# Kernel tuning notes

Hardware: AMD Instinct MI355X
Metric: run time of the kernel (lower is better)

The kernel has to match this reference:

```python
import jax, jax.numpy as jnp
import numpy as np

M1 = 16
M2 = 16

def _spectral_conv(x, w1c, w2c):
    # x: [B,C,H,W] real; w*c: [C,C,M1,M2] complex
    B, C, H, W = x.shape
    xft = jnp.fft.rfft2(x)                      # [B,C,H,W//2+1]
    top = jnp.einsum('bixy,ioxy->boxy', xft[:, :, :M1, :M2], w1c)
    bot = jnp.einsum('bixy,ioxy->boxy', xft[:, :, -M1:, :M2], w2c)
    out_ft = jnp.zeros((B, w1c.shape[1], H, W // 2 + 1), dtype=xft.dtype)
    out_ft = out_ft.at[:, :, :M1, :M2].set(top)
    out_ft = out_ft.at[:, :, -M1:, :M2].set(bot)
    return jnp.fft.irfft2(out_ft, s=(H, W))

def _fourier_layer(x, w1c, w2c, cw, cb):
    x1 = _spectral_conv(x, w1c, w2c)
    x2 = jnp.einsum('bchw,oc->bohw', x, cw) + cb[None, :, None, None]  # 1x1 conv
    return jax.nn.gelu(x1 + x2, approximate=False)

def setup_inputs() -> dict:
    key = jax.random.key(0)
    ks = jax.random.split(key, 12)
    B, H, W, Tin, C, step = 8, 256, 256, 10, 32, 5
    scale = 1.0 / (C * C)
    return {
        'x': jax.random.normal(ks[0], (B, H, W, Tin), dtype=jnp.float32),
        'fc0_w': jax.random.normal(ks[1], (Tin + 2, C), dtype=jnp.float32) * 0.1,
        'fc0_b': jax.random.normal(ks[2], (C,), dtype=jnp.float32) * 0.1,
        'w1': jax.random.uniform(ks[3], (6, C, C, M1, M2, 2), dtype=jnp.float32) * scale,
        'w2': jax.random.uniform(ks[4], (6, C, C, M1, M2, 2), dtype=jnp.float32) * scale,
        'conv_w': jax.random.normal(ks[5], (6, C, C), dtype=jnp.float32) * 0.1,
        'conv_b': jax.random.normal(ks[6], (6, C), dtype=jnp.float32) * 0.1,
        'fc1_w': jax.random.normal(ks[7], (C, 128), dtype=jnp.float32) * 0.1,
        'fc1_b': jax.random.normal(ks[8], (128,), dtype=jnp.float32) * 0.1,
        'fc2_w': jax.random.normal(ks[9], (128, step), dtype=jnp.float32) * 0.1,
        'fc2_b': jax.random.normal(ks[10], (step,), dtype=jnp.float32) * 0.1,
    }

def reference(x, fc0_w, fc0_b, w1, w2, conv_w, conv_b, fc1_w, fc1_b, fc2_w, fc2_b):
    B, H, W, _ = x.shape
    gridx = jnp.broadcast_to(jnp.linspace(0.0, 1.0, H, dtype=x.dtype)[None, :, None, None], (B, H, W, 1))
    gridy = jnp.broadcast_to(jnp.linspace(0.0, 1.0, W, dtype=x.dtype)[None, None, :, None], (B, H, W, 1))
    h = jnp.concatenate([x, gridx, gridy], axis=-1)          # [B,H,W,T_in+2]
    h = jnp.einsum('bhwc,cd->bhwd', h, fc0_w) + fc0_b        # lift
    h = jnp.transpose(h, (0, 3, 1, 2))                        # [B,C,H,W]
    w1c = jax.lax.complex(w1[..., 0], w1[..., 1])
    w2c = jax.lax.complex(w2[..., 0], w2[..., 1])
    f = lambda z, i: _fourier_layer(z, w1c[i], w2c[i], conv_w[i], conv_b[i])
    h0 = f(h, 0)
    h = f(h, 1)
    h = f(h, 2) + h0
    h1 = f(h, 3)
    h = f(h, 4)
    h = f(h, 5) + h1
    h = jnp.transpose(h, (0, 2, 3, 1))                        # [B,H,W,C]
    h = jax.nn.gelu(jnp.einsum('bhwc,cd->bhwd', h, fc1_w) + fc1_b, approximate=False)
    return jnp.einsum('bhwc,cd->bhwd', h, fc2_w) + fc2_b      # [B,H,W,step]
```

## Files before the change

### kernel.cpp

```cpp
#include <hip/hip_runtime.h>
#include <math.h>

#define C_ 32
#define H_ 256
#define W_ 256
#define HW_ 65536
#define CHW_ 2097152
#define TWO_PI 6.28318530717958647692f

typedef __bf16 bf16x8 __attribute__((ext_vector_type(8)));
typedef float  f32x4  __attribute__((ext_vector_type(4)));

__device__ __forceinline__ bf16x8 as_bf16x8(uint4 u) {
    return __builtin_bit_cast(bf16x8, u);
}
__device__ __forceinline__ unsigned short bfbits(__bf16 h) {
    return __builtin_bit_cast(unsigned short, h);
}
__device__ __forceinline__ bf16x8 mk8(unsigned a, unsigned b, unsigned c, unsigned d) {
    return __builtin_bit_cast(bf16x8, make_uint4(a, b, c, d));
}
__device__ __forceinline__ unsigned rot16(unsigned v) { return (v >> 16) | (v << 16); }
__device__ __forceinline__ uint2 splitpack(float x, float y) {
    __bf16 xh = (__bf16)x, yh = (__bf16)y;
    float xl = x - (float)xh, yl = y - (float)yh;
    unsigned hi = (unsigned)bfbits(xh) | ((unsigned)bfbits(yh) << 16);
    unsigned lo = (unsigned)bfbits((__bf16)xl) | ((unsigned)bfbits((__bf16)yl) << 16);
    return make_uint2(hi, lo);
}

__device__ __forceinline__ float gelu_exact(float x) {
    return 0.5f * x * (1.0f + erff(x * 0.7071067811865475f));
}

__global__ void k_probe(float* __restrict__ out, float ws_kib) {
    if (threadIdx.x == 0 && blockIdx.x == 0) out[0] = ws_kib;
}

__global__ __launch_bounds__(256)
void k_twprep(unsigned short* __restrict__ twfg, uint2* __restrict__ twbfg,
              float2* __restrict__ twg) {
    int f = blockIdx.x * 256 + threadIdx.x;
    {
        int i  = f & 7;
        int c  = (f >> 3) & 15;
        int g  = (f >> 7) & 3;
        int nt = (f >> 9) & 1;
        int kk = f >> 10;
        int k  = kk * 32 + 8 * g + i;
        int a  = (k * c) & 255;
        float ang = (float)a * (TWO_PI / 256.0f);
        float s_, c_; sincosf(ang, &s_, &c_);
        float val = nt ? -s_ : c_;
        __bf16 hi = (__bf16)val;
        __bf16 lo = (__bf16)(val - (float)hi);
        twfg[f]        = bfbits(hi);
        twfg[8192 + f] = bfbits(lo);
    }
    if (f < 256) {
        float a = TWO_PI * (1.0f / 256.0f) * (float)f;
        float s_, c_; sincosf(a, &s_, &c_);
        twbfg[f] = splitpack(c_, s_);
        twg[f]   = make_float2(c_, s_);
    }
}

__global__ __launch_bounds__(256)
void k_lift(const float* __restrict__ xb, const float* __restrict__ fc0_w,
            const float* __restrict__ fc0_b, float* __restrict__ out) {
    __shared__ float wsh[12 * 32];
    __shared__ float bsh[32];
    int tid = threadIdx.x;
    for (int n = tid; n < 384; n += 256) wsh[n] = fc0_w[n];
    if (tid < 32) bsh[tid] = fc0_b[tid];
    __syncthreads();
    int p = blockIdx.x * 256 + tid;
    int w = p & 255;
    int h = (p >> 8) & 255;
    float in[12];
    const float* xp = xb + (size_t)p * 10;
    #pragma unroll
    for (int t = 0; t < 10; ++t) in[t] = xp[t];
    in[10] = (float)h * (1.0f / 255.0f);
    in[11] = (float)w * (1.0f / 255.0f);
    float* op = out + (p & 0xFFFF) + (size_t)(p >> 16) * CHW_;
    #pragma unroll
    for (int c = 0; c < 32; ++c) {
        float acc = bsh[c];
        #pragma unroll
        for (int t = 0; t < 12; ++t) acc += in[t] * wsh[t * 32 + c];
        op[(size_t)c * HW_] = acc;
    }
}

__global__ __launch_bounds__(512)
void k_dftw_dfth(const float* __restrict__ X, float* __restrict__ G,
                 const unsigned short* __restrict__ twfg,
                 const uint2* __restrict__ twbfg) {
    __shared__ __align__(16) unsigned short twf[16384];
    __shared__ uint2 twbf[256];
    __shared__ uint2 slp[256][17];
    int tid = threadIdx.x;
    {
        const uint4* tf4 = (const uint4*)twfg;
        uint4* tw4 = (uint4*)twf;
        #pragma unroll
        for (int f = tid; f < 2048; f += 512) tw4[f] = tf4[f];
        if (tid < 256) twbf[tid] = twbfg[tid];
    }
    __syncthreads();
    int wv = tid >> 6, lane = tid & 63, kg = lane >> 4, cl = lane & 15;
    const uint4* twp = (const uint4*)twf;
    int bo = blockIdx.x;
    const float* xp = X + (size_t)bo * HW_;
    #pragma unroll
    for (int tt = 0; tt < 2; ++tt) {
        int t = wv * 2 + tt;
        const float* xr = xp + (size_t)(t * 16 + cl) * 256 + 8 * kg;
        f32x4 acc0 = {0.f, 0.f, 0.f, 0.f};
        f32x4 acc1 = {0.f, 0.f, 0.f, 0.f};
        #pragma unroll
        for (int kk = 0; kk < 8; ++kk) {
            float4 a0 = *(const float4*)(xr + kk * 32);
            float4 a1 = *(const float4*)(xr + kk * 32 + 4);
            float xv[8] = {a0.x, a0.y, a0.z, a0.w, a1.x, a1.y, a1.z, a1.w};
            bf16x8 Ah, Al;
            #pragma unroll
            for (int i = 0; i < 8; ++i) {
                __bf16 h = (__bf16)xv[i];
                Ah[i] = h;
                Al[i] = (__bf16)(xv[i] - (float)h);
            }
            int base = kk * 128 + kg * 16 + cl;
            bf16x8 Bh0 = as_bf16x8(twp[base]);
            bf16x8 Bh1 = as_bf16x8(twp[base + 64]);
            bf16x8 Bl0 = as_bf16x8(twp[base + 1024]);
            bf16x8 Bl1 = as_bf16x8(twp[base + 1088]);
            acc0 = __builtin_amdgcn_mfma_f32_16x16x32_bf16(Al, Bl0, acc0, 0, 0, 0);
            acc0 = __builtin_amdgcn_mfma_f32_16x16x32_bf16(Ah, Bl0, acc0, 0, 0, 0);
            acc0 = __builtin_amdgcn_mfma_f32_16x16x32_bf16(Al, Bh0, acc0, 0, 0, 0);
            acc0 = __builtin_amdgcn_mfma_f32_16x16x32_bf16(Ah, Bh0, acc0, 0, 0, 0);
            acc1 = __builtin_amdgcn_mfma_f32_16x16x32_bf16(Al, Bl1, acc1, 0, 0, 0);
            acc1 = __builtin_amdgcn_mfma_f32_16x16x32_bf16(Ah, Bl1, acc1, 0, 0, 0);
            acc1 = __builtin_amdgcn_mfma_f32_16x16x32_bf16(Al, Bh1, acc1, 0, 0, 0);
            acc1 = __builtin_amdgcn_mfma_f32_16x16x32_bf16(Ah, Bh1, acc1, 0, 0, 0);
        }
        #pragma unroll
        for (int q = 0; q < 4; ++q)
            slp[t * 16 + 4 * kg + q][cl] = splitpack(acc0[q], acc1[q]);
    }
    __syncthreads();
    if (wv < 4) {
        int mt = wv >> 1, nt = wv & 1;
        int kyi_row = mt * 16 + cl;
        int ky = (kyi_row < 16) ? kyi_row : (kyi_row + 224);
        f32x4 acc = {0.f, 0.f, 0.f, 0.f};
        #pragma unroll 4
        for (int kk = 0; kk < 16; ++kk) {
            unsigned Ah[4], Al[4], Bh[4], Bl[4];
            #pragma unroll
            for (int j2 = 0; j2 < 4; ++j2) {
                int h = kk * 16 + kg * 4 + j2;
                uint2 t = twbf[(ky * h) & 255];
                Ah[j2] = t.x; Al[j2] = t.y;
                uint2 d = slp[h][cl];
                if (nt == 0) { Bh[j2] = d.x;                       Bl[j2] = d.y; }
                else         { Bh[j2] = rot16(d.x) ^ 0x80000000u;  Bl[j2] = rot16(d.y) ^ 0x80000000u; }
            }
            bf16x8 ah = mk8(Ah[0], Ah[1], Ah[2], Ah[3]);
            bf16x8 al = mk8(Al[0], Al[1], Al[2], Al[3]);
            bf16x8 bh = mk8(Bh[0], Bh[1], Bh[2], Bh[3]);
            bf16x8 bl = mk8(Bl[0], Bl[1], Bl[2], Bl[3]);
            acc = __builtin_amdgcn_mfma_f32_16x16x32_bf16(al, bl, acc, 0, 0, 0);
            acc = __builtin_amdgcn_mfma_f32_16x16x32_bf16(ah, bl, acc, 0, 0, 0);
            acc = __builtin_amdgcn_mfma_f32_16x16x32_bf16(al, bh, acc, 0, 0, 0);
            acc = __builtin_amdgcn_mfma_f32_16x16x32_bf16(ah, bh, acc, 0, 0, 0);
        }
        float* gf = G + (((size_t)bo * 512 + (size_t)(mt * 16 + 4 * kg) * 16 + cl) * 2 + nt);
        #pragma unroll
        for (int q = 0; q < 4; ++q) gf[q * 32] = acc[q];
    }
}

__global__ __launch_bounds__(256)
void k_mix_idfth(const float* __restrict__ G, const float* __restrict__ w1,
                 const float* __restrict__ w2, float* __restrict__ T,
                 const uint2* __restrict__ twbfg) {
    __shared__ uint2 twbf[256];
    __shared__ uint2 gre[32][17];
    __shared__ uint2 gim[32][17];
    int tid = threadIdx.x;
    twbf[tid] = twbfg[tid];
    int bo = blockIdx.x;
    int b = bo >> 5, o = bo & 31;
    {
        int kyi = tid >> 4, kx = tid & 15;
        const float2* gp1 = (const float2*)G + (size_t)b * 16384 + (size_t)kyi * 16 + kx;
        const float2* gp2 = gp1 + 256;
        const float2* wv1 = (const float2*)w1 + (((size_t)o) * 16 + kyi) * 16 + kx;
        const float2* wv2 = (const float2*)w2 + (((size_t)o) * 16 + kyi) * 16 + kx;
        float ar1 = 0.f, ai1 = 0.f, ar2 = 0.f, ai2 = 0.f;
        #pragma unroll
        for (int i = 0; i < 32; ++i) {
            float2 g1 = gp1[(size_t)i * 512];
            float2 g2 = gp2[(size_t)i * 512];
            float2 wa = wv1[(size_t)i * 8192];
            float2 wb = wv2[(size_t)i * 8192];
            ar1 += g1.x * wa.x - g1.y * wa.y;
            ai1 += g1.x * wa.y + g1.y * wa.x;
            ar2 += g2.x * wb.x - g2.y * wb.y;
            ai2 += g2.x * wb.y + g2.y * wb.x;
        }
        gre[kyi][kx]      = splitpack(ar1, -ai1);
        gim[kyi][kx]      = splitpack(ai1,  ar1);
        gre[kyi + 16][kx] = splitpack(ar2, -ai2);
        gim[kyi + 16][kx] = splitpack(ai2,  ar2);
    }
    __syncthreads();
    int wv = tid >> 6, lane = tid & 63, kg = lane >> 4, cl = lane & 15;
    f32x4 accR[4] = {{0,0,0,0},{0,0,0,0},{0,0,0,0},{0,0,0,0}};
    f32x4 accI[4] = {{0,0,0,0},{0,0,0,0},{0,0,0,0},{0,0,0,0}};
    #pragma unroll
    for (int kk = 0; kk < 2; ++kk) {
        unsigned Brh[4], Brl[4], Bih[4], Bil[4];
        #pragma unroll
        for (int j2 = 0; j2 < 4; ++j2) {
            int kyi = kk * 16 + 4 * kg + j2;
            uint2 dr = gre[kyi][cl]; Brh[j2] = dr.x; Brl[j2] = dr.y;
            uint2 di = gim[kyi][cl]; Bih[j2] = di.x; Bil[j2] = di.y;
        }
        bf16x8 brh = mk8(Brh[0], Brh[1], Brh[2], Brh[3]);
        bf16x8 brl = mk8(Brl[0], Brl[1], Brl[2], Brl[3]);
        bf16x8 bih = mk8(Bih[0], Bih[1], Bih[2], Bih[3]);
        bf16x8 bil = mk8(Bil[0], Bil[1], Bil[2], Bil[3]);
        #pragma unroll
        for (int m = 0; m < 4; ++m) {
            int h = (wv * 4 + m) * 16 + cl;
            unsigned Ah[4], Al[4];
            #pragma unroll
            for (int j2 = 0; j2 < 4; ++j2) {
                int kyi = kk * 16 + 4 * kg + j2;
                int ky  = (kk == 0) ? kyi : (kyi + 224);
                uint2 t = twbf[(ky * h) & 255];
                Ah[j2] = t.x; Al[j2] = t.y;
            }
            bf16x8 ah = mk8(Ah[0], Ah[1], Ah[2], Ah[3]);
            bf16x8 al = mk8(Al[0], Al[1], Al[2], Al[3]);
            accR[m] = __builtin_amdgcn_mfma_f32_16x16x32_bf16(al, brl, accR[m], 0, 0, 0);
            accR[m] = __builtin_amdgcn_mfma_f32_16x16x32_bf16(ah, brl, accR[m], 0, 0, 0);
            accR[m] = __builtin_amdgcn_mfma_f32_16x16x32_bf16(al, brh, accR[m], 0, 0, 0);
            accR[m] = __builtin_amdgcn_mfma_f32_16x16x32_bf16(ah, brh, accR[m], 0, 0, 0);
            accI[m] = __builtin_amdgcn_mfma_f32_16x16x32_bf16(al, bil, accI[m], 0, 0, 0);
            accI[m] = __builtin_amdgcn_mfma_f32_16x16x32_bf16(ah, bil, accI[m], 0, 0, 0);
            accI[m] = __builtin_amdgcn_mfma_f32_16x16x32_bf16(al, bih, accI[m], 0, 0, 0);
            accI[m] = __builtin_amdgcn_mfma_f32_16x16x32_bf16(ah, bih, accI[m], 0, 0, 0);
        }
    }
    float sc = (cl == 0 ? 1.0f : 2.0f) * (1.0f / 65536.0f);
    float2* tp = (float2*)T;
    #pragma unroll
    for (int m = 0; m < 4; ++m) {
        #pragma unroll
        for (int q = 0; q < 4; ++q) {
            int h = (wv * 4 + m) * 16 + 4 * kg + q;
            tp[((size_t)bo * 256 + h) * 16 + cl] =
                make_float2(accR[m][q] * sc, accI[m][q] * sc);
        }
    }
}

__global__ __launch_bounds__(256)
void k_invw_conv(const float* __restrict__ T, const float* X,
                 const float* __restrict__ cw, const float* __restrict__ cb,
                 const float* __restrict__ skip, float* Y,
                 const float2* __restrict__ twg) {
    __shared__ float2 tw[256];
    __shared__ float2 tsh[32][17];
    int tid = threadIdx.x;
    tw[tid] = twg[tid];
    int b  = blockIdx.x >> 8;
    int hh = blockIdx.x & 255;
    const float2* tp = (const float2*)T;
    for (int n = tid; n < 512; n += 256) {
        int o = n >> 4, kx = n & 15;
        tsh[o][kx] = tp[(((size_t)(b * 32 + o)) * 256 + hh) * 16 + kx];
    }
    __syncthreads();
    int wv = tid >> 6, lane = tid & 63;
    int kg = lane >> 4, cl = lane & 15;

    bf16x8 Ash[2], Asl[2];
    bf16x8 Ach[2], Acl2[2];
    #pragma unroll
    for (int mt = 0; mt < 2; ++mt) {
        int o = mt * 16 + cl;
        const float4* cwp = (const float4*)(cw + o * 32 + 8 * kg);
        float4 c0 = cwp[0], c1 = cwp[1];
        float cvv[8] = {c0.x, c0.y, c0.z, c0.w, c1.x, c1.y, c1.z, c1.w};
        #pragma unroll
        for (int j = 0; j < 8; ++j) {
            int k = 8 * kg + j;
            float2 tv = tsh[o][k >> 1];
            float v = (k & 1) ? -tv.y : tv.x;
            __bf16 hv = (__bf16)v;
            Ash[mt][j] = hv;
            Asl[mt][j] = (__bf16)(v - (float)hv);
            float cv = cvv[j];
            __bf16 hc = (__bf16)cv;
            Ach[mt][j]  = hc;
            Acl2[mt][j] = (__bf16)(cv - (float)hc);
        }
    }

    f32x4 acc[2][4];
    #pragma unroll
    for (int mt = 0; mt < 2; ++mt)
        #pragma unroll
        for (int nt = 0; nt < 4; ++nt)
            #pragma unroll
            for (int q = 0; q < 4; ++q)
                acc[mt][nt][q] = cb[mt * 16 + 4 * kg + q];

    const float* xb = X + (size_t)b * CHW_ + (size_t)hh * W_;
    #pragma unroll
    for (int nt = 0; nt < 4; ++nt) {
        int w = 64 * wv + 16 * nt + cl;
        bf16x8 Bth, Btl, Bxh, Bxl;
        #pragma unroll
        for (int j = 0; j < 8; ++j) {
            int k = 8 * kg + j;
            float2 cs = tw[((k >> 1) * w) & 255];
            float v = (k & 1) ? cs.y : cs.x;
            __bf16 hv = (__bf16)v;
            Bth[j] = hv;
            Btl[j] = (__bf16)(v - (float)hv);
            float xv = xb[(size_t)k * HW_ + w];
            __bf16 hx = (__bf16)xv;
            Bxh[j] = hx;
            Bxl[j] = (__bf16)(xv - (float)hx);
        }
        #pragma unroll
        for (int mt = 0; mt < 2; ++mt) {
            acc[mt][nt] = __builtin_amdgcn_mfma_f32_16x16x32_bf16(Asl[mt],  Btl, acc[mt][nt], 0, 0, 0);
            acc[mt][nt] = __builtin_amdgcn_mfma_f32_16x16x32_bf16(Ash[mt],  Btl, acc[mt][nt], 0, 0, 0);
            acc[mt][nt] = __builtin_amdgcn_mfma_f32_16x16x32_bf16(Asl[mt],  Bth, acc[mt][nt], 0, 0, 0);
            acc[mt][nt] = __builtin_amdgcn_mfma_f32_16x16x32_bf16(Ash[mt],  Bth, acc[mt][nt], 0, 0, 0);
            acc[mt][nt] = __builtin_amdgcn_mfma_f32_16x16x32_bf16(Acl2[mt], Bxl, acc[mt][nt], 0, 0, 0);
            acc[mt][nt] = __builtin_amdgcn_mfma_f32_16x16x32_bf16(Ach[mt],  Bxl, acc[mt][nt], 0, 0, 0);
            acc[mt][nt] = __builtin_amdgcn_mfma_f32_16x16x32_bf16(Acl2[mt], Bxh, acc[mt][nt], 0, 0, 0);
            acc[mt][nt] = __builtin_amdgcn_mfma_f32_16x16x32_bf16(Ach[mt],  Bxh, acc[mt][nt], 0, 0, 0);
        }
    }

    const bool hasSkip = (skip != nullptr);
    #pragma unroll
    for (int mt = 0; mt < 2; ++mt) {
        #pragma unroll
        for (int q = 0; q < 4; ++q) {
            int o = 16 * mt + 4 * kg + q;
            size_t rowbase = (size_t)b * CHW_ + (size_t)o * HW_ + (size_t)hh * W_;
            #pragma unroll
            for (int nt = 0; nt < 4; ++nt) {
                int w = 64 * wv + 16 * nt + cl;
                float g = gelu_exact(acc[mt][nt][q]);
                if (hasSkip) g += skip[rowbase + w];
                Y[rowbase + w] = g;
            }
        }
    }
}

__global__ __launch_bounds__(256)
void k_w1prep(const float* __restrict__ fc1_w, uint2* __restrict__ w1g) {
    int f = blockIdx.x * 256 + threadIdx.x;
    int j2 = f & 3, cl = (f >> 2) & 15, kg = (f >> 6) & 3, nt = f >> 8;
    int d = nt * 16 + cl, k0 = 8 * kg + 2 * j2;
    w1g[f] = splitpack(fc1_w[k0 * 128 + d], fc1_w[(k0 + 1) * 128 + d]);
}

__global__ __launch_bounds__(256)
void k_mlp(const float* __restrict__ X, const uint2* __restrict__ w1g,
           const float* __restrict__ fc1_b, const float* __restrict__ fc2_w,
           const float* __restrict__ fc2_b, float* __restrict__ outb, int nChunks) {
    __shared__ float bsh[128];
    __shared__ float w2sh[640];
    __shared__ float Gsh[64][133];
    int tid = threadIdx.x;
    if (tid < 128) bsh[tid] = fc1_b[tid];
    for (int f = tid; f < 640; f += 256) w2sh[f] = fc2_w[f];
    float b2[5];
    #pragma unroll
    for (int s = 0; s < 5; ++s) b2[s] = fc2_b[s];
    int wv = tid >> 6, lane = tid & 63, kg = lane >> 4, cl = lane & 15;
    int ploc2 = tid >> 2, dq = tid & 3;
    __syncthreads();
    float xr[8];
    {
        int c0 = blockIdx.x;
        if (c0 < nChunks) {
            int P0 = c0 * 64;
            const float* xp = X + (size_t)(P0 >> 16) * CHW_ + (size_t)(8 * kg) * HW_
                            + ((P0 & 0xFFFF) + wv * 16 + cl);
            #pragma unroll
            for (int j = 0; j < 8; ++j) xr[j] = xp[(size_t)j * HW_];
        }
    }
    for (int chunk = blockIdx.x; chunk < nChunks; chunk += gridDim.x) {
        int P0 = chunk * 64;
        bf16x8 Ah, Al;
        #pragma unroll
        for (int j = 0; j < 8; ++j) {
            float v = xr[j];
            __bf16 h = (__bf16)v;
            Ah[j] = h;
            Al[j] = (__bf16)(v - (float)h);
        }
        int nc = chunk + gridDim.x;
        if (nc < nChunks) {
            int P1 = nc * 64;
            const float* xp = X + (size_t)(P1 >> 16) * CHW_ + (size_t)(8 * kg) * HW_
                            + ((P1 & 0xFFFF) + wv * 16 + cl);
            #pragma unroll
            for (int j = 0; j < 8; ++j) xr[j] = xp[(size_t)j * HW_];
        }
        #pragma unroll
        for (int nt = 0; nt < 8; ++nt) {
            const uint2* wp = &w1g[((nt * 4 + kg) * 16 + cl) * 4];
            uint2 q0 = wp[0], q1 = wp[1], q2 = wp[2], q3 = wp[3];
            bf16x8 Bh = mk8(q0.x, q1.x, q2.x, q3.x);
            bf16x8 Bl = mk8(q0.y, q1.y, q2.y, q3.y);
            float bv = bsh[nt * 16 + cl];
            f32x4 acc = {bv, bv, bv, bv};
            acc = __builtin_amdgcn_mfma_f32_16x16x32_bf16(Al, Bl, acc, 0, 0, 0);
            acc = __builtin_amdgcn_mfma_f32_16x16x32_bf16(Ah, Bl, acc, 0, 0, 0);
            acc = __builtin_amdgcn_mfma_f32_16x16x32_bf16(Al, Bh, acc, 0, 0, 0);
            acc = __builtin_amdgcn_mfma_f32_16x16x32_bf16(Ah, Bh, acc, 0, 0, 0);
            #pragma unroll
            for (int q = 0; q < 4; ++q)
                Gsh[wv * 16 + 4 * kg + q][nt * 16 + cl] = gelu_exact(acc[q]);
        }
        __syncthreads();
        {
            float a5[5] = {0.f, 0.f, 0.f, 0.f, 0.f};
            #pragma unroll 8
            for (int j = 0; j < 32; ++j) {
                int d = dq + 4 * j;
                float gv = Gsh[ploc2][d];
                #pragma unroll
                for (int s = 0; s < 5; ++s) a5[s] += gv * w2sh[d * 5 + s];
            }
            #pragma unroll
            for (int s = 0; s < 5; ++s) {
                a5[s] += __shfl_xor(a5[s], 1);
                a5[s] += __shfl_xor(a5[s], 2);
            }
            if (dq == 0) {
                float* op = outb + (size_t)(P0 + ploc2) * 5;
                #pragma unroll
                for (int s = 0; s < 5; ++s) op[s] = a5[s] + b2[s];
            }
        }
        __syncthreads();
    }
}

extern "C" void kernel_launch(void* const* d_in, const int* in_sizes, int n_in,
                              void* d_out, int out_size, void* d_ws, size_t ws_size,
                              hipStream_t stream) {
    const float* x      = (const float*)d_in[0];
    const float* fc0_w  = (const float*)d_in[1];
    const float* fc0_b  = (const float*)d_in[2];
    const float* w1     = (const float*)d_in[3];
    const float* w2     = (const float*)d_in[4];
    const float* conv_w = (const float*)d_in[5];
    const float* conv_b = (const float*)d_in[6];
    const float* fc1_w  = (const float*)d_in[7];
    const float* fc1_b  = (const float*)d_in[8];
    const float* fc2_w  = (const float*)d_in[9];
    const float* fc2_b  = (const float*)d_in[10];
    float* out = (float*)d_out;

    const size_t ACTb = 16777216;
    const size_t ACTi = 2097152;
    const size_t STb = 2097152, Gb = 262144;
    const size_t STi = 262144,  Gi = 32768;

    if (ws_size >= 2 * ACTb * sizeof(float)) {
        float* A0 = (float*)d_ws;
        float* A1 = A0 + ACTb;
        float* ST = out;
        float* G  = ST + STb;
        float* TBL = G + Gb;
        unsigned short* twfg = (unsigned short*)TBL;
        uint2* twbfg = (uint2*)(TBL + 8192);
        float2* twg  = (float2*)(TBL + 8704);

        k_twprep<<<32, 256, 0, stream>>>(twfg, twbfg, twg);
        k_lift<<<2048, 256, 0, stream>>>(x, fc0_w, fc0_b, A0);
        auto layer = [&](int l, const float* Xin, float* Yout, const float* skip) {
            k_dftw_dfth<<<256, 512, 0, stream>>>(Xin, G, twfg, twbfg);
            k_mix_idfth<<<256, 256, 0, stream>>>(G, w1 + (size_t)l * 524288,
                                                 w2 + (size_t)l * 524288, ST, twbfg);
            k_invw_conv<<<2048, 256, 0, stream>>>(ST, Xin, conv_w + (size_t)l * 1024,
                                                  conv_b + (size_t)l * 32, skip, Yout,
                                                  twg);
        };
        layer(0, A0, A1, nullptr);
        layer(1, A0, A0, nullptr);
        layer(2, A0, A0, A1);
        layer(3, A0, A1, nullptr);
        layer(4, A0, A0, nullptr);
        layer(5, A0, A0, A1);
        k_w1prep<<<8, 256, 0, stream>>>(fc1_w, (uint2*)A1);
        k_mlp<<<2048, 256, 0, stream>>>(A0, (const uint2*)A1, fc1_b, fc2_w, fc2_b,
                                        out, 8192);

    } else if (ws_size >= (3 * ACTi + STi + 2 * Gi) * sizeof(float)) {
        float* A0 = (float*)d_ws;
        float* A1 = A0 + ACTi;
        float* A2 = A1 + ACTi;
        float* ST = A2 + ACTi;
        float* G  = ST + STi;
        float* TBL = G + Gi;
        unsigned short* twfg = (unsigned short*)TBL;
        uint2* twbfg = (uint2*)(TBL + 8192);
        float2* twg  = (float2*)(TBL + 8704);

        k_twprep<<<32, 256, 0, stream>>>(twfg, twbfg, twg);
        auto layer = [&](int l, const float* Xin, float* Yout, const float* skip) {
            k_dftw_dfth<<<32, 512, 0, stream>>>(Xin, G, twfg, twbfg);
            k_mix_idfth<<<32, 256, 0, stream>>>(G, w1 + (size_t)l * 524288,
                                                w2 + (size_t)l * 524288, ST, twbfg);
            k_invw_conv<<<256, 256, 0, stream>>>(ST, Xin, conv_w + (size_t)l * 1024,
                                                 conv_b + (size_t)l * 32, skip, Yout,
                                                 twg);
        };
        for (int b = 0; b < 8; ++b) {
            k_lift<<<256, 256, 0, stream>>>(x + (size_t)b * HW_ * 10, fc0_w, fc0_b, A0);
            layer(0, A0, A2, nullptr);
            layer(1, A0, A1, nullptr);
            layer(2, A1, A0, A2);
            layer(3, A0, A2, nullptr);
            layer(4, A0, A1, nullptr);
            layer(5, A1, A0, A2);
            k_w1prep<<<8, 256, 0, stream>>>(fc1_w, (uint2*)ST);
            k_mlp<<<1024, 256, 0, stream>>>(A0, (const uint2*)ST, fc1_b, fc2_w,
                                            fc2_b, out + (size_t)b * 327680, 1024);
        }
    } else {
        k_probe<<<1, 64, 0, stream>>>(out, (float)(ws_size >> 10));
    }
}
```

Measured before the change: 545.2 us.

## Store activations as split bf16 hi/lo planes instead of fp32

Activations between layers are now stored as two separate bf16 planes (high and residual low parts) rather than fp32. Consumers load the pre-split halves directly into MFMA operands instead of splitting on the fly in every kernel that reads them. Total bytes stay the same, but the conversion work moves from each of several readers to the single writer. The cost is two separate strided stores and loads per element, and 16-bit scattered accesses in the conv and MLP kernels may coalesce less well.

```diff
diff --git a/kernel.cpp b/kernel.cpp
--- a/kernel.cpp
+++ b/kernel.cpp
@@ -16,6 +16,9 @@
 }
 __device__ __forceinline__ unsigned short bfbits(__bf16 h) {
     return __builtin_bit_cast(unsigned short, h);
+}
+__device__ __forceinline__ __bf16 bfval(unsigned short u) {
+    return __builtin_bit_cast(__bf16, u);
 }
 __device__ __forceinline__ bf16x8 mk8(unsigned a, unsigned b, unsigned c, unsigned d) {
     return __builtin_bit_cast(bf16x8, make_uint4(a, b, c, d));
@@ -67,7 +70,8 @@
 
 __global__ __launch_bounds__(256)
 void k_lift(const float* __restrict__ xb, const float* __restrict__ fc0_w,
-            const float* __restrict__ fc0_b, float* __restrict__ out) {
+            const float* __restrict__ fc0_b, unsigned short* __restrict__ out,
+            int ae) {
     __shared__ float wsh[12 * 32];
     __shared__ float bsh[32];
     int tid = threadIdx.x;
@@ -83,18 +87,23 @@
     for (int t = 0; t < 10; ++t) in[t] = xp[t];
     in[10] = (float)h * (1.0f / 255.0f);
     in[11] = (float)w * (1.0f / 255.0f);
-    float* op = out + (p & 0xFFFF) + (size_t)(p >> 16) * CHW_;
+    size_t base = (size_t)(p & 0xFFFF) + (size_t)(p >> 16) * CHW_;
+    unsigned short* oh = out + base;
+    unsigned short* ol = out + (size_t)ae + base;
     #pragma unroll
     for (int c = 0; c < 32; ++c) {
         float acc = bsh[c];
         #pragma unroll
         for (int t = 0; t < 12; ++t) acc += in[t] * wsh[t * 32 + c];
-        op[(size_t)c * HW_] = acc;
+        __bf16 hb = (__bf16)acc;
+        oh[(size_t)c * HW_] = bfbits(hb);
+        ol[(size_t)c * HW_] = bfbits((__bf16)(acc - (float)hb));
     }
 }
 
 __global__ __launch_bounds__(512)
-void k_dftw_dfth(const float* __restrict__ X, float* __restrict__ G,
+void k_dftw_dfth(const unsigned short* __restrict__ X, int ae,
+                 float* __restrict__ G,
                  const unsigned short* __restrict__ twfg,
                  const uint2* __restrict__ twbfg) {
     __shared__ __align__(16) unsigned short twf[16384];
@@ -112,25 +121,18 @@
     int wv = tid >> 6, lane = tid & 63, kg = lane >> 4, cl = lane & 15;
     const uint4* twp = (const uint4*)twf;
     int bo = blockIdx.x;
-    const float* xp = X + (size_t)bo * HW_;
+    const unsigned short* xh = X + (size_t)bo * HW_;
+    const unsigned short* xl = X + (size_t)ae + (size_t)bo * HW_;
     #pragma unroll
     for (int tt = 0; tt < 2; ++tt) {
         int t = wv * 2 + tt;
-        const float* xr = xp + (size_t)(t * 16 + cl) * 256 + 8 * kg;
+        size_t rowb = (size_t)(t * 16 + cl) * 256 + 8 * kg;
         f32x4 acc0 = {0.f, 0.f, 0.f, 0.f};
         f32x4 acc1 = {0.f, 0.f, 0.f, 0.f};
         #pragma unroll
         for (int kk = 0; kk < 8; ++kk) {
-            float4 a0 = *(const float4*)(xr + kk * 32);
-            float4 a1 = *(const float4*)(xr + kk * 32 + 4);
-            float xv[8] = {a0.x, a0.y, a0.z, a0.w, a1.x, a1.y, a1.z, a1.w};
-            bf16x8 Ah, Al;
-            #pragma unroll
-            for (int i = 0; i < 8; ++i) {
-                __bf16 h = (__bf16)xv[i];
-                Ah[i] = h;
-                Al[i] = (__bf16)(xv[i] - (float)h);
-            }
+            bf16x8 Ah = as_bf16x8(*(const uint4*)(xh + rowb + kk * 32));
+            bf16x8 Al = as_bf16x8(*(const uint4*)(xl + rowb + kk * 32));
             int base = kk * 128 + kg * 16 + cl;
             bf16x8 Bh0 = as_bf16x8(twp[base]);
             bf16x8 Bh1 = as_bf16x8(twp[base + 64]);
@@ -270,9 +272,9 @@
 }
 
 __global__ __launch_bounds__(256)
-void k_invw_conv(const float* __restrict__ T, const float* X,
+void k_invw_conv(const float* __restrict__ T, const unsigned short* X, int ae,
                  const float* __restrict__ cw, const float* __restrict__ cb,
-                 const float* __restrict__ skip, float* Y,
+                 const unsigned short* __restrict__ skip, unsigned short* Y,
                  const float2* __restrict__ twg) {
     __shared__ float2 tw[256];
     __shared__ float2 tsh[32][17];
@@ -321,7 +323,8 @@
             for (int q = 0; q < 4; ++q)
                 acc[mt][nt][q] = cb[mt * 16 + 4 * kg + q];
 
-    const float* xb = X + (size_t)b * CHW_ + (size_t)hh * W_;
+    const unsigned short* xbh = X + (size_t)b * CHW_ + (size_t)hh * W_;
+    const unsigned short* xbl = xbh + (size_t)ae;
     #pragma unroll
     for (int nt = 0; nt < 4; ++nt) {
         int w = 64 * wv + 16 * nt + cl;
@@ -334,10 +337,9 @@
             __bf16 hv = (__bf16)v;
             Bth[j] = hv;
             Btl[j] = (__bf16)(v - (float)hv);
-            float xv = xb[(size_t)k * HW_ + w];
-            __bf16 hx = (__bf16)xv;
-            Bxh[j] = hx;
-            Bxl[j] = (__bf16)(xv - (float)hx);
+            size_t xi = (size_t)k * HW_ + w;
+            Bxh[j] = bfval(xbh[xi]);
+            Bxl[j] = bfval(xbl[xi]);
         }
         #pragma unroll
         for (int mt = 0; mt < 2; ++mt) {
@@ -362,9 +364,13 @@
             #pragma unroll
             for (int nt = 0; nt < 4; ++nt) {
                 int w = 64 * wv + 16 * nt + cl;
+                size_t idx = rowbase + w;
                 float g = gelu_exact(acc[mt][nt][q]);
-                if (hasSkip) g += skip[rowbase + w];
-                Y[rowbase + w] = g;
+                if (hasSkip)
+                    g += (float)bfval(skip[idx]) + (float)bfval(skip[(size_t)ae + idx]);
+                __bf16 gh = (__bf16)g;
+                Y[idx]              = bfbits(gh);
+                Y[(size_t)ae + idx] = bfbits((__bf16)(g - (float)gh));
             }
         }
     }
@@ -379,7 +385,8 @@
 }
 
 __global__ __launch_bounds__(256)
-void k_mlp(const float* __restrict__ X, const uint2* __restrict__ w1g,
+void k_mlp(const unsigned short* __restrict__ X, int ae,
+           const uint2* __restrict__ w1g,
            const float* __restrict__ fc1_b, const float* __restrict__ fc2_w,
            const float* __restrict__ fc2_b, float* __restrict__ outb, int nChunks) {
     __shared__ float bsh[128];
@@ -394,15 +401,18 @@
     int wv = tid >> 6, lane = tid & 63, kg = lane >> 4, cl = lane & 15;
     int ploc2 = tid >> 2, dq = tid & 3;
     __syncthreads();
-    float xr[8];
+    unsigned short xrh[8], xrl[8];
     {
         int c0 = blockIdx.x;
         if (c0 < nChunks) {
             int P0 = c0 * 64;
-            const float* xp = X + (size_t)(P0 >> 16) * CHW_ + (size_t)(8 * kg) * HW_
-                            + ((P0 & 0xFFFF) + wv * 16 + cl);
-            #pragma unroll
-            for (int j = 0; j < 8; ++j) xr[j] = xp[(size_t)j * HW_];
+            const unsigned short* xp = X + (size_t)(P0 >> 16) * CHW_
+                + (size_t)(8 * kg) * HW_ + ((P0 & 0xFFFF) + wv * 16 + cl);
+            #pragma unroll
+            for (int j = 0; j < 8; ++j) {
+                xrh[j] = xp[(size_t)j * HW_];
+                xrl[j] = xp[(size_t)ae + (size_t)j * HW_];
+            }
         }
     }
     for (int chunk = blockIdx.x; chunk < nChunks; chunk += gridDim.x) {
@@ -410,18 +420,19 @@
         bf16x8 Ah, Al;
         #pragma unroll
         for (int j = 0; j < 8; ++j) {
-            float v = xr[j];
-            __bf16 h = (__bf16)v;
-            Ah[j] = h;
-            Al[j] = (__bf16)(v - (float)h);
+            Ah[j] = bfval(xrh[j]);
+            Al[j] = bfval(xrl[j]);
         }
         int nc = chunk + gridDim.x;
         if (nc < nChunks) {
             int P1 = nc * 64;
-            const float* xp = X + (size_t)(P1 >> 16) * CHW_ + (size_t)(8 * kg) * HW_
-                            + ((P1 & 0xFFFF) + wv * 16 + cl);
-            #pragma unroll
-            for (int j = 0; j < 8; ++j) xr[j] = xp[(size_t)j * HW_];
+            const unsigned short* xp = X + (size_t)(P1 >> 16) * CHW_
+                + (size_t)(8 * kg) * HW_ + ((P1 & 0xFFFF) + wv * 16 + cl);
+            #pragma unroll
+            for (int j = 0; j < 8; ++j) {
+                xrh[j] = xp[(size_t)j * HW_];
+                xrl[j] = xp[(size_t)ae + (size_t)j * HW_];
+            }
         }
         #pragma unroll
         for (int nt = 0; nt < 8; ++nt) {
@@ -486,8 +497,8 @@
     const size_t STi = 262144,  Gi = 32768;
 
     if (ws_size >= 2 * ACTb * sizeof(float)) {
-        float* A0 = (float*)d_ws;
-        float* A1 = A0 + ACTb;
+        unsigned short* A0u = (unsigned short*)d_ws;
+        unsigned short* A1u = A0u + 2 * ACTb;
         float* ST = out;
         float* G  = ST + STb;
         float* TBL = G + Gb;
@@ -496,30 +507,32 @@
         float2* twg  = (float2*)(TBL + 8704);
 
         k_twprep<<<32, 256, 0, stream>>>(twfg, twbfg, twg);
-        k_lift<<<2048, 256, 0, stream>>>(x, fc0_w, fc0_b, A0);
-        auto layer = [&](int l, const float* Xin, float* Yout, const float* skip) {
-            k_dftw_dfth<<<256, 512, 0, stream>>>(Xin, G, twfg, twbfg);
+        k_lift<<<2048, 256, 0, stream>>>(x, fc0_w, fc0_b, A0u, (int)ACTb);
+        auto layer = [&](int l, const unsigned short* Xin, unsigned short* Yout,
+                         const unsigned short* skip) {
+            k_dftw_dfth<<<256, 512, 0, stream>>>(Xin, (int)ACTb, G, twfg, twbfg);
             k_mix_idfth<<<256, 256, 0, stream>>>(G, w1 + (size_t)l * 524288,
                                                  w2 + (size_t)l * 524288, ST, twbfg);
-            k_invw_conv<<<2048, 256, 0, stream>>>(ST, Xin, conv_w + (size_t)l * 1024,
+            k_invw_conv<<<2048, 256, 0, stream>>>(ST, Xin, (int)ACTb,
+                                                  conv_w + (size_t)l * 1024,
                                                   conv_b + (size_t)l * 32, skip, Yout,
                                                   twg);
         };
-        layer(0, A0, A1, nullptr);
-        layer(1, A0, A0, nullptr);
-        layer(2, A0, A0, A1);
-        layer(3, A0, A1, nullptr);
-        layer(4, A0, A0, nullptr);
-        layer(5, A0, A0, A1);
-        k_w1prep<<<8, 256, 0, stream>>>(fc1_w, (uint2*)A1);
-        k_mlp<<<2048, 256, 0, stream>>>(A0, (const uint2*)A1, fc1_b, fc2_w, fc2_b,
-                                        out, 8192);
+        layer(0, A0u, A1u, nullptr);
+        layer(1, A0u, A0u, nullptr);
+        layer(2, A0u, A0u, A1u);
+        layer(3, A0u, A1u, nullptr);
+        layer(4, A0u, A0u, nullptr);
+        layer(5, A0u, A0u, A1u);
+        k_w1prep<<<8, 256, 0, stream>>>(fc1_w, (uint2*)A1u);
+        k_mlp<<<2048, 256, 0, stream>>>(A0u, (int)ACTb, (const uint2*)A1u,
+                                        fc1_b, fc2_w, fc2_b, out, 8192);
 
     } else if (ws_size >= (3 * ACTi + STi + 2 * Gi) * sizeof(float)) {
-        float* A0 = (float*)d_ws;
-        float* A1 = A0 + ACTi;
-        float* A2 = A1 + ACTi;
-        float* ST = A2 + ACTi;
+        unsigned short* A0u = (unsigned short*)d_ws;
+        unsigned short* A1u = A0u + 2 * ACTi;
+        unsigned short* A2u = A0u + 4 * ACTi;
+        float* ST = (float*)(A0u + 6 * ACTi);
         float* G  = ST + STi;
         float* TBL = G + Gi;
         unsigned short* twfg = (unsigned short*)TBL;
@@ -527,25 +540,29 @@
         float2* twg  = (float2*)(TBL + 8704);
 
         k_twprep<<<32, 256, 0, stream>>>(twfg, twbfg, twg);
-        auto layer = [&](int l, const float* Xin, float* Yout, const float* skip) {
-            k_dftw_dfth<<<32, 512, 0, stream>>>(Xin, G, twfg, twbfg);
+        auto layer = [&](int l, const unsigned short* Xin, unsigned short* Yout,
+                         const unsigned short* skip) {
+            k_dftw_dfth<<<32, 512, 0, stream>>>(Xin, (int)ACTi, G, twfg, twbfg);
             k_mix_idfth<<<32, 256, 0, stream>>>(G, w1 + (size_t)l * 524288,
                                                 w2 + (size_t)l * 524288, ST, twbfg);
-            k_invw_conv<<<256, 256, 0, stream>>>(ST, Xin, conv_w + (size_t)l * 1024,
+            k_invw_conv<<<256, 256, 0, stream>>>(ST, Xin, (int)ACTi,
+                                                 conv_w + (size_t)l * 1024,
                                                  conv_b + (size_t)l * 32, skip, Yout,
                                                  twg);
         };
         for (int b = 0; b < 8; ++b) {
-            k_lift<<<256, 256, 0, stream>>>(x + (size_t)b * HW_ * 10, fc0_w, fc0_b, A0);
-            layer(0, A0, A2, nullptr);
-            layer(1, A0, A1, nullptr);
-            layer(2, A1, A0, A2);
-            layer(3, A0, A2, nullptr);
-            layer(4, A0, A1, nullptr);
-            layer(5, A1, A0, A2);
+            k_lift<<<256, 256, 0, stream>>>(x + (size_t)b * HW_ * 10, fc0_w, fc0_b,
+                                            A0u, (int)ACTi);
+            layer(0, A0u, A2u, nullptr);
+            layer(1, A0u, A1u, nullptr);
+            layer(2, A1u, A0u, A2u);
+            layer(3, A0u, A2u, nullptr);
+            layer(4, A0u, A1u, nullptr);
+            layer(5, A1u, A0u, A2u);
             k_w1prep<<<8, 256, 0, stream>>>(fc1_w, (uint2*)ST);
-            k_mlp<<<1024, 256, 0, stream>>>(A0, (const uint2*)ST, fc1_b, fc2_w,
-                                            fc2_b, out + (size_t)b * 327680, 1024);
+            k_mlp<<<1024, 256, 0, stream>>>(A0u, (int)ACTi, (const uint2*)ST,
+                                            fc1_b, fc2_w, fc2_b,
+                                            out + (size_t)b * 327680, 1024);
         }
     } else {
         k_probe<<<1, 64, 0, stream>>>(out, (float)(ws_size >> 10));
```

Measured after the change: 601.2 us. 10.3% more time.

## Switch activation layout from BCHW to BHCW across lift, DFT, pointwise, projection

Applied to the files above, without the earlier changes.

Changes the activation storage from [B,C,H,W] to [B,H,C,W] so that all 32 channels for a given row sit contiguously in one 32 KB slab. Every kernel that reads or writes activations (lift, the W-direction DFT, the pointwise conv+GELU, and the projection head) has its addressing updated. The aim is better locality: channel-strided accesses become 1 KB apart instead of 256 KB, which should reduce TLB and DRAM page pressure. Kernels that index by channel-plane, such as the DFT block mapping bo→(b,c), now read rows strided by 32 KB, which could hurt their coalescing.

```diff
diff --git a/kernel.cpp b/kernel.cpp
--- a/kernel.cpp
+++ b/kernel.cpp
@@ -6,7 +6,9 @@
 #define W_ 256
 #define HW_ 65536
 #define CHW_ 2097152
+#define HCW_ 8192
 #define TWO_PI 6.28318530717958647692f
+
 
 typedef __bf16 bf16x8 __attribute__((ext_vector_type(8)));
 typedef float  f32x4  __attribute__((ext_vector_type(4)));
@@ -83,13 +85,13 @@
     for (int t = 0; t < 10; ++t) in[t] = xp[t];
     in[10] = (float)h * (1.0f / 255.0f);
     in[11] = (float)w * (1.0f / 255.0f);
-    float* op = out + (p & 0xFFFF) + (size_t)(p >> 16) * CHW_;
+    float* op = out + (size_t)(p >> 16) * CHW_ + (size_t)h * HCW_ + w;
     #pragma unroll
     for (int c = 0; c < 32; ++c) {
         float acc = bsh[c];
         #pragma unroll
         for (int t = 0; t < 12; ++t) acc += in[t] * wsh[t * 32 + c];
-        op[(size_t)c * HW_] = acc;
+        op[c * 256] = acc;
     }
 }
 
@@ -112,11 +114,11 @@
     int wv = tid >> 6, lane = tid & 63, kg = lane >> 4, cl = lane & 15;
     const uint4* twp = (const uint4*)twf;
     int bo = blockIdx.x;
-    const float* xp = X + (size_t)bo * HW_;
+    const float* xp = X + (size_t)(bo >> 5) * CHW_ + (size_t)(bo & 31) * 256;
     #pragma unroll
     for (int tt = 0; tt < 2; ++tt) {
         int t = wv * 2 + tt;
-        const float* xr = xp + (size_t)(t * 16 + cl) * 256 + 8 * kg;
+        const float* xr = xp + (size_t)(t * 16 + cl) * HCW_ + 8 * kg;
         f32x4 acc0 = {0.f, 0.f, 0.f, 0.f};
         f32x4 acc1 = {0.f, 0.f, 0.f, 0.f};
         #pragma unroll
@@ -321,7 +323,7 @@
             for (int q = 0; q < 4; ++q)
                 acc[mt][nt][q] = cb[mt * 16 + 4 * kg + q];
 
-    const float* xb = X + (size_t)b * CHW_ + (size_t)hh * W_;
+    const float* xb = X + (size_t)b * CHW_ + (size_t)hh * HCW_;
     #pragma unroll
     for (int nt = 0; nt < 4; ++nt) {
         int w = 64 * wv + 16 * nt + cl;
@@ -334,7 +336,7 @@
             __bf16 hv = (__bf16)v;
             Bth[j] = hv;
             Btl[j] = (__bf16)(v - (float)hv);
-            float xv = xb[(size_t)k * HW_ + w];
+            float xv = xb[k * 256 + w];
             __bf16 hx = (__bf16)xv;
             Bxh[j] = hx;
             Bxl[j] = (__bf16)(xv - (float)hx);
@@ -353,12 +355,13 @@
     }
 
     const bool hasSkip = (skip != nullptr);
+    size_t slab = (size_t)b * CHW_ + (size_t)hh * HCW_;
     #pragma unroll
     for (int mt = 0; mt < 2; ++mt) {
         #pragma unroll
         for (int q = 0; q < 4; ++q) {
             int o = 16 * mt + 4 * kg + q;
-            size_t rowbase = (size_t)b * CHW_ + (size_t)o * HW_ + (size_t)hh * W_;
+            size_t rowbase = slab + (size_t)o * 256;
             #pragma unroll
             for (int nt = 0; nt < 4; ++nt) {
                 int w = 64 * wv + 16 * nt + cl;
@@ -399,10 +402,12 @@
         int c0 = blockIdx.x;
         if (c0 < nChunks) {
             int P0 = c0 * 64;
-            const float* xp = X + (size_t)(P0 >> 16) * CHW_ + (size_t)(8 * kg) * HW_
-                            + ((P0 & 0xFFFF) + wv * 16 + cl);
-            #pragma unroll
-            for (int j = 0; j < 8; ++j) xr[j] = xp[(size_t)j * HW_];
+            int hw0 = P0 & 0xFFFF;
+            const float* xp = X + (size_t)(P0 >> 16) * CHW_
+                + (size_t)(hw0 >> 8) * HCW_ + (8 * kg) * 256
+                + ((hw0 & 255) + wv * 16 + cl);
+            #pragma unroll
+            for (int j = 0; j < 8; ++j) xr[j] = xp[j * 256];
         }
     }
     for (int chunk = blockIdx.x; chunk < nChunks; chunk += gridDim.x) {
@@ -418,10 +423,12 @@
         int nc = chunk + gridDim.x;
         if (nc < nChunks) {
             int P1 = nc * 64;
-            const float* xp = X + (size_t)(P1 >> 16) * CHW_ + (size_t)(8 * kg) * HW_
-                            + ((P1 & 0xFFFF) + wv * 16 + cl);
-            #pragma unroll
-            for (int j = 0; j < 8; ++j) xr[j] = xp[(size_t)j * HW_];
+            int hw1 = P1 & 0xFFFF;
+            const float* xp = X + (size_t)(P1 >> 16) * CHW_
+                + (size_t)(hw1 >> 8) * HCW_ + (8 * kg) * 256
+                + ((hw1 & 255) + wv * 16 + cl);
+            #pragma unroll
+            for (int j = 0; j < 8; ++j) xr[j] = xp[j * 256];
         }
         #pragma unroll
         for (int nt = 0; nt < 8; ++nt) {
```

Result: no change. 541.6 us (-0.7%).
